# Kernel tuning notes

Hardware: AMD Instinct MI355X
Metric: run time of the kernel (lower is better)

The kernel has to match this reference:

```python
import jax, jax.numpy as jnp
import numpy as np

N = 100000      # num nodes
E = 800000      # num edges
IN = 256        # in_features
D = 64          # out_features per head
H = 4           # num_heads
EF = 64         # edge_feats
NET = 8         # num_etype
SLOPE = 0.2     # leaky relu negative slope


def setup_inputs() -> dict:
    key = jax.random.key(0)
    ks = jax.random.split(key, 12)
    s = 0.05
    h = jax.random.normal(ks[0], (N, IN), jnp.float32)
    row = jax.random.randint(ks[1], (E,), 0, N, dtype=jnp.int32)   # src
    col = jax.random.randint(ks[2], (E,), 0, N, dtype=jnp.int32)   # dst
    tp = jax.random.randint(ks[3], (E,), 0, NET, dtype=jnp.int32)  # edge type
    W = jax.random.normal(ks[4], (IN, D * H), jnp.float32) * s
    W_e = jax.random.normal(ks[5], (EF, EF * H), jnp.float32) * s
    edge_emb = jax.random.normal(ks[6], (NET, EF), jnp.float32) * s
    a_l = jax.random.normal(ks[7], (1, H, D), jnp.float32) * s
    a_r = jax.random.normal(ks[8], (1, H, D), jnp.float32) * s
    a_e = jax.random.normal(ks[9], (1, H, EF), jnp.float32) * s
    res_W = jax.random.normal(ks[10], (IN, D * H), jnp.float32) * s
    res_b = jnp.zeros((D * H,), jnp.float32)
    return {"h": h, "W": W, "W_e": W_e, "edge_emb": edge_emb,
            "a_l": a_l, "a_r": a_r, "a_e": a_e,
            "res_W": res_W, "res_b": res_b,
            "row": row, "col": col, "tp": tp}


def reference(h, W, W_e, edge_emb, a_l, a_r, a_e, res_W, res_b, row, col, tp):
    # node projection -> [N, H, D]; nan-guard as in the original
    emb = jnp.nan_to_num((h @ W).reshape(-1, H, D), nan=0.0)
    # edge-type embedding projection -> [NET, H, EF]
    e = (edge_emb @ W_e).reshape(-1, H, EF)
    # per-edge attention logits [E, H]
    h_l = (a_l * emb).sum(-1)[row]
    h_r = (a_r * emb).sum(-1)[col]
    h_e = (a_e * e).sum(-1)[tp]
    att = jax.nn.leaky_relu(h_l + h_r + h_e, SLOPE)
    # segment softmax over edges grouped by destination node
    m = jax.ops.segment_max(att, col, num_segments=N)          # [N, H]
    ex = jnp.exp(att - m[col])                                 # [E, H]
    denom = jax.ops.segment_sum(ex, col, num_segments=N)      # [N, H]
    alpha = ex / denom[col]                                    # [E, H]
    # gather-multiply-scatter message passing: [E, H, D] -> [N, H, D]
    msg = emb[row] * alpha[:, :, None]
    out = jax.ops.segment_sum(msg, col, num_segments=N).reshape(N, H * D)
    # residual linear + elu activation
    out = out + h @ res_W + res_b
    return jax.nn.elu(out)
```

## Files before the change

kernel.cpp:

```cpp
#include <hip/hip_runtime.h>

#define N_NODES 100000
#define E_EDGES 800000
#define IN_F 256
#define D_HEAD 64
#define H_HEADS 4
#define EF_F 64
#define NET_T 8
#define HD 256
#define SLOPE 0.2f
#define NTILES ((N_NODES + 63) / 64)

typedef unsigned short u16;
typedef unsigned long long u64;
typedef __attribute__((ext_vector_type(8))) short bf16x8;
typedef __attribute__((ext_vector_type(4))) float f32x4;

static __device__ __forceinline__ u16 f2bf(float f) {
    unsigned int u = __float_as_uint(f);
    unsigned int r = u + 0x7FFFu + ((u >> 16) & 1u);
    return (u16)(r >> 16);
}
static __device__ __forceinline__ float bf2f(unsigned int u) {
    return __uint_as_float(u << 16);
}

__global__ void k_se(const float* __restrict__ edge_emb, const float* __restrict__ W_e,
                     const float* __restrict__ a_e, float* __restrict__ s_e) {
    int tid = threadIdx.x;
    int t  = tid >> 5;
    int h  = (tid >> 3) & 3;
    int fc = tid & 7;
    float part = 0.f;
    for (int j = 0; j < 8; ++j) {
        int f = fc * 8 + j;
        float acc = 0.f;
        for (int k = 0; k < EF_F; ++k)
            acc += edge_emb[t * EF_F + k] * W_e[k * (EF_F * H_HEADS) + h * EF_F + f];
        part += a_e[h * EF_F + f] * acc;
    }
    for (int off = 1; off < 8; off <<= 1)
        part += __shfl_xor(part, off, 64);
    if (fc == 0) s_e[t * H_HEADS + h] = part;
}

__global__ void k_prep_w(const float* __restrict__ W, const float* __restrict__ resW,
                         u16* __restrict__ Bfrag) {
    const int gid = blockIdx.x * 256 + threadIdx.x;
    const int lane = gid & 63;
    const int fragid = gid >> 6;
    const int n = fragid & 3;
    const int ks = (fragid >> 2) & 7;
    const int g = fragid >> 5;
    const int c = g * 64 + n * 16 + (lane & 15);
    const int k0 = ks * 32 + (lane >> 4) * 8;
    const float* src = (c < HD) ? &W[c] : &resW[c - HD];
    u16 tmp[8];
#pragma unroll
    for (int j = 0; j < 8; ++j)
        tmp[j] = f2bf(src[(size_t)(k0 + j) * HD]);
    *reinterpret_cast<uint4*>(&Bfrag[(size_t)fragid * 512 + lane * 8]) =
        *reinterpret_cast<const uint4*>(tmp);
}

__global__ __launch_bounds__(512, 2)
void k_mfma(const float* __restrict__ A, const u16* __restrict__ Bfrag,
            const float* __restrict__ a_l, const float* __restrict__ a_r,
            const float* __restrict__ resb,
            u16* __restrict__ emb_bf, float* __restrict__ s_l, float* __restrict__ s_r,
            float* __restrict__ outp) {
    __shared__ char At[32768];
    const int tid = threadIdx.x;
    const int lane = tid & 63;
    const int wid = tid >> 6;
    const int row0 = blockIdx.x * 64;

#pragma unroll
    for (int c = 0; c < 8; ++c) {
        const int lin8 = c * 4096 + tid * 8;
        const int r_lin = lin8 >> 9;
        int grow = row0 + r_lin;
        if (grow >= N_NODES) grow = N_NODES - 1;
        const int colb = lin8 & 511;
        const float4 v = *reinterpret_cast<const float4*>(&A[(size_t)grow * IN_F + (colb >> 1)]);
        uint2 o;
        o.x = (unsigned)f2bf(v.x) | ((unsigned)f2bf(v.y) << 16);
        o.y = (unsigned)f2bf(v.z) | ((unsigned)f2bf(v.w) << 16);
        *reinterpret_cast<uint2*>(&At[lin8 ^ ((r_lin & 7) << 4)]) = o;
    }
    __syncthreads();

    const int lr = lane & 15;
    const int lg = lane >> 4;
    const int xr = (lr & 7) << 4;
    const int klg = lg * 16;

    int rowbase[4];
#pragma unroll
    for (int m = 0; m < 4; ++m) rowbase[m] = (m * 16 + lr) * 512;

    const u16* bp = Bfrag + (size_t)wid * 16384 + lane * 8;

    f32x4 acc[4][4] = {};
#pragma unroll
    for (int ks = 0; ks < 8; ++ks) {
        bf16x8 af[4], bfr[4];
        const int kx = ((ks << 6) + klg) ^ xr;
#pragma unroll
        for (int n = 0; n < 4; ++n)
            bfr[n] = *reinterpret_cast<const bf16x8*>(&bp[ks * 2048 + n * 512]);
#pragma unroll
        for (int m = 0; m < 4; ++m)
            af[m] = *reinterpret_cast<const bf16x8*>(&At[rowbase[m] + kx]);
#pragma unroll
        for (int m = 0; m < 4; ++m)
#pragma unroll
            for (int n = 0; n < 4; ++n)
                acc[m][n] = __builtin_amdgcn_mfma_f32_16x16x32_bf16(bfr[n], af[m], acc[m][n], 0, 0, 0);
    }

    if (wid < 4) {
        const int h = wid;
        float4 alv[4], arv[4];
#pragma unroll
        for (int n = 0; n < 4; ++n) {
            alv[n] = *reinterpret_cast<const float4*>(&a_l[h * D_HEAD + n * 16 + lg * 4]);
            arv[n] = *reinterpret_cast<const float4*>(&a_r[h * D_HEAD + n * 16 + lg * 4]);
        }
#pragma unroll
        for (int m = 0; m < 4; ++m) {
            const int node = row0 + m * 16 + lr;
            float dl = 0.f, dr = 0.f;
            u64 pk[4];
#pragma unroll
            for (int n = 0; n < 4; ++n) {
                float v0 = acc[m][n][0], v1 = acc[m][n][1], v2 = acc[m][n][2], v3 = acc[m][n][3];
                v0 = isnan(v0) ? 0.f : v0;
                v1 = isnan(v1) ? 0.f : v1;
                v2 = isnan(v2) ? 0.f : v2;
                v3 = isnan(v3) ? 0.f : v3;
                dl += v0 * alv[n].x + v1 * alv[n].y + v2 * alv[n].z + v3 * alv[n].w;
                dr += v0 * arv[n].x + v1 * arv[n].y + v2 * arv[n].z + v3 * arv[n].w;
                pk[n] = (u64)f2bf(v0) | ((u64)f2bf(v1) << 16) |
                        ((u64)f2bf(v2) << 32) | ((u64)f2bf(v3) << 48);
            }
            if (node < N_NODES) {
                const size_t base = (size_t)node * HD + h * D_HEAD + lg * 4;
#pragma unroll
                for (int n = 0; n < 4; ++n)
                    *reinterpret_cast<u64*>(&emb_bf[base + n * 16]) = pk[n];
            }
            dl += __shfl_xor(dl, 16, 64); dr += __shfl_xor(dr, 16, 64);
            dl += __shfl_xor(dl, 32, 64); dr += __shfl_xor(dr, 32, 64);
            if (lg == 0 && node < N_NODES) {
                s_l[node * H_HEADS + h] = dl;
                s_r[node * H_HEADS + h] = dr;
            }
        }
    } else {
        const int c0 = (wid - 4) * 64 + lg * 4;
        float4 rb[4];
#pragma unroll
        for (int n = 0; n < 4; ++n)
            rb[n] = *reinterpret_cast<const float4*>(&resb[c0 + n * 16]);
#pragma unroll
        for (int m = 0; m < 4; ++m) {
            const int node = row0 + m * 16 + lr;
            if (node < N_NODES) {
                const size_t base = (size_t)node * HD + c0;
#pragma unroll
                for (int n = 0; n < 4; ++n) {
                    float4 o;
                    o.x = acc[m][n][0] + rb[n].x;
                    o.y = acc[m][n][1] + rb[n].y;
                    o.z = acc[m][n][2] + rb[n].z;
                    o.w = acc[m][n][3] + rb[n].w;
                    *reinterpret_cast<float4*>(&outp[base + n * 16]) = o;
                }
            }
        }
    }
}

__global__ void k_hist(const int* __restrict__ col, int* __restrict__ counts) {
    int e = blockIdx.x * 256 + threadIdx.x;
    if (e < E_EDGES) atomicAdd(&counts[col[e]], 1);
}

__global__ void k_scan1(const int* __restrict__ counts, int* __restrict__ row_ptr,
                        int* __restrict__ partials) {
    __shared__ int sd[256];
    const int t = threadIdx.x, b = blockIdx.x;
    const int base = b * 1024 + t * 4;
    int v[4];
#pragma unroll
    for (int j = 0; j < 4; ++j) v[j] = (base + j < N_NODES) ? counts[base + j] : 0;
    const int s = v[0] + v[1] + v[2] + v[3];
    sd[t] = s;
    __syncthreads();
    for (int off = 1; off < 256; off <<= 1) {
        int y = (t >= off) ? sd[t - off] : 0;
        __syncthreads();
        sd[t] += y;
        __syncthreads();
    }
    int p = sd[t] - s;
#pragma unroll
    for (int j = 0; j < 4; ++j) {
        if (base + j < N_NODES) row_ptr[base + j] = p;
        p += v[j];
    }
    if (t == 255) partials[b] = sd[255];
}

__global__ void k_scan2(int* __restrict__ partials) {
    __shared__ int sd[128];
    const int t = threadIdx.x;
    const int v = (t < 98) ? partials[t] : 0;
    sd[t] = v;
    __syncthreads();
    for (int off = 1; off < 128; off <<= 1) {
        int y = (t >= off) ? sd[t - off] : 0;
        __syncthreads();
        sd[t] += y;
        __syncthreads();
    }
    if (t < 98) partials[t] = sd[t] - v;
}

__global__ void k_scan3(int* __restrict__ row_ptr, int* __restrict__ fill,
                        const int* __restrict__ partials) {
    const int i = blockIdx.x * 256 + threadIdx.x;
    if (i < N_NODES) {
        const int v = row_ptr[i] + partials[i >> 10];
        row_ptr[i] = v;
        fill[i] = v;
    }
    if (i == 0) row_ptr[N_NODES] = E_EDGES;
}

__global__ void k_scatter(const int* __restrict__ row, const int* __restrict__ col,
                          const int* __restrict__ tp, const float* __restrict__ s_l,
                          const float* __restrict__ s_r, const float* __restrict__ s_e,
                          int* __restrict__ fill, int* __restrict__ perm_row,
                          float4* __restrict__ exw_perm) {
    const int e = blockIdx.x * 256 + threadIdx.x;
    if (e >= E_EDGES) return;
    const int r = row[e], c = col[e], t = tp[e];
    const float4 sl = *reinterpret_cast<const float4*>(&s_l[r * 4]);
    const float4 sr = *reinterpret_cast<const float4*>(&s_r[c * 4]);
    const float4 se = *reinterpret_cast<const float4*>(&s_e[t * 4]);
    float4 ex;
    float x;
    x = sl.x + sr.x + se.x; x = (x > 0.f) ? x : SLOPE * x; ex.x = __expf(x);
    x = sl.y + sr.y + se.y; x = (x > 0.f) ? x : SLOPE * x; ex.y = __expf(x);
    x = sl.z + sr.z + se.z; x = (x > 0.f) ? x : SLOPE * x; ex.z = __expf(x);
    x = sl.w + sr.w + se.w; x = (x > 0.f) ? x : SLOPE * x; ex.w = __expf(x);
    const int p = atomicAdd(&fill[c], 1);
    perm_row[p] = r;
    exw_perm[p] = ex;
}

__global__ __launch_bounds__(256)
void k_aggregate(const int* __restrict__ row_ptr, const int* __restrict__ perm_row,
                 const float* __restrict__ exw_perm,
                 const u16* __restrict__ emb_bf, float* __restrict__ outp) {
    const int wave = threadIdx.x >> 6;
    const int lane = threadIdx.x & 63;
    const int n = blockIdx.x * 4 + wave;
    const int h = lane >> 4;
    const int start = row_ptr[n], end = row_ptr[n + 1];
    const size_t o = (size_t)n * HD + lane * 4;
    const float4 res = *reinterpret_cast<const float4*>(&outp[o]);

    float a0 = 0.f, a1 = 0.f, a2 = 0.f, a3 = 0.f, den = 0.f;
    int i = start;
    for (; i + 4 <= end; i += 4) {
        const int r0 = perm_row[i],     r1 = perm_row[i + 1];
        const int r2 = perm_row[i + 2], r3 = perm_row[i + 3];
        const float ex0 = exw_perm[(i)     * 4 + h];
        const float ex1 = exw_perm[(i + 1) * 4 + h];
        const float ex2 = exw_perm[(i + 2) * 4 + h];
        const float ex3 = exw_perm[(i + 3) * 4 + h];
        const u64 ev0 = *reinterpret_cast<const u64*>(&emb_bf[(size_t)r0 * HD + lane * 4]);
        const u64 ev1 = *reinterpret_cast<const u64*>(&emb_bf[(size_t)r1 * HD + lane * 4]);
        const u64 ev2 = *reinterpret_cast<const u64*>(&emb_bf[(size_t)r2 * HD + lane * 4]);
        const u64 ev3 = *reinterpret_cast<const u64*>(&emb_bf[(size_t)r3 * HD + lane * 4]);
        a0 += ex0 * bf2f((unsigned)(ev0) & 0xFFFFu)       + ex1 * bf2f((unsigned)(ev1) & 0xFFFFu)
            + ex2 * bf2f((unsigned)(ev2) & 0xFFFFu)       + ex3 * bf2f((unsigned)(ev3) & 0xFFFFu);
        a1 += ex0 * bf2f((unsigned)(ev0 >> 16) & 0xFFFFu) + ex1 * bf2f((unsigned)(ev1 >> 16) & 0xFFFFu)
            + ex2 * bf2f((unsigned)(ev2 >> 16) & 0xFFFFu) + ex3 * bf2f((unsigned)(ev3 >> 16) & 0xFFFFu);
        a2 += ex0 * bf2f((unsigned)(ev0 >> 32) & 0xFFFFu) + ex1 * bf2f((unsigned)(ev1 >> 32) & 0xFFFFu)
            + ex2 * bf2f((unsigned)(ev2 >> 32) & 0xFFFFu) + ex3 * bf2f((unsigned)(ev3 >> 32) & 0xFFFFu);
        a3 += ex0 * bf2f((unsigned)(ev0 >> 48) & 0xFFFFu) + ex1 * bf2f((unsigned)(ev1 >> 48) & 0xFFFFu)
            + ex2 * bf2f((unsigned)(ev2 >> 48) & 0xFFFFu) + ex3 * bf2f((unsigned)(ev3 >> 48) & 0xFFFFu);
        den += ex0 + ex1 + ex2 + ex3;
    }
    for (; i < end; ++i) {
        const int r0 = perm_row[i];
        const float ex0 = exw_perm[i * 4 + h];
        const u64 ev0 = *reinterpret_cast<const u64*>(&emb_bf[(size_t)r0 * HD + lane * 4]);
        a0 += ex0 * bf2f((unsigned)(ev0) & 0xFFFFu);
        a1 += ex0 * bf2f((unsigned)(ev0 >> 16) & 0xFFFFu);
        a2 += ex0 * bf2f((unsigned)(ev0 >> 32) & 0xFFFFu);
        a3 += ex0 * bf2f((unsigned)(ev0 >> 48) & 0xFFFFu);
        den += ex0;
    }
    const float inv = (den > 0.f) ? 1.f / den : 0.f;
    float4 out;
    float x;
    x = a0 * inv + res.x; out.x = (x > 0.f) ? x : __expf(x) - 1.f;
    x = a1 * inv + res.y; out.y = (x > 0.f) ? x : __expf(x) - 1.f;
    x = a2 * inv + res.z; out.z = (x > 0.f) ? x : __expf(x) - 1.f;
    x = a3 * inv + res.w; out.w = (x > 0.f) ? x : __expf(x) - 1.f;
    *reinterpret_cast<float4*>(&outp[o]) = out;
}

extern "C" void kernel_launch(void* const* d_in, const int* in_sizes, int n_in,
                              void* d_out, int out_size, void* d_ws, size_t ws_size,
                              hipStream_t stream) {
    const float* h    = (const float*)d_in[0];
    const float* W    = (const float*)d_in[1];
    const float* W_e  = (const float*)d_in[2];
    const float* eemb = (const float*)d_in[3];
    const float* a_l  = (const float*)d_in[4];
    const float* a_r  = (const float*)d_in[5];
    const float* a_e  = (const float*)d_in[6];
    const float* resW = (const float*)d_in[7];
    const float* resb = (const float*)d_in[8];
    const int* row = (const int*)d_in[9];
    const int* col = (const int*)d_in[10];
    const int* tp  = (const int*)d_in[11];
    float* outp = (float*)d_out;

    char* ws = (char*)d_ws;
    size_t off = 0;
    auto alloc = [&](size_t b) { size_t o = off; off += (b + 255) & ~(size_t)255; return o; };
    u16*  Bfrag   = (u16*)(ws + alloc((size_t)512 * IN_F * 2));
    u16*  emb_bf  = (u16*)(ws + alloc((size_t)N_NODES * HD * 2));
    float* s_l    = (float*)(ws + alloc((size_t)N_NODES * H_HEADS * 4));
    float* s_r    = (float*)(ws + alloc((size_t)N_NODES * H_HEADS * 4));
    float* s_e    = (float*)(ws + alloc(NET_T * H_HEADS * 4));
    int*  counts  = (int*)(ws + alloc((size_t)N_NODES * 4));
    int*  row_ptr = (int*)(ws + alloc((size_t)(N_NODES + 1) * 4));
    int*  fill    = (int*)(ws + alloc((size_t)N_NODES * 4));
    int*  perm_row= (int*)(ws + alloc((size_t)E_EDGES * 4));
    float* exw_perm=(float*)(ws + alloc((size_t)E_EDGES * H_HEADS * 4));
    int*  partials= (int*)(ws + alloc(128 * 4));

    k_se<<<1, 256, 0, stream>>>(eemb, W_e, a_e, s_e);
    k_prep_w<<<64, 256, 0, stream>>>(W, resW, Bfrag);
    k_mfma<<<NTILES, 512, 0, stream>>>(h, Bfrag, a_l, a_r, resb, emb_bf, s_l, s_r, outp);
    hipMemsetAsync(counts, 0, (size_t)N_NODES * 4, stream);
    k_hist<<<(E_EDGES + 255) / 256, 256, 0, stream>>>(col, counts);
    k_scan1<<<98, 256, 0, stream>>>(counts, row_ptr, partials);
    k_scan2<<<1, 128, 0, stream>>>(partials);
    k_scan3<<<(N_NODES + 255) / 256, 256, 0, stream>>>(row_ptr, fill, partials);
    k_scatter<<<(E_EDGES + 255) / 256, 256, 0, stream>>>(row, col, tp, s_l, s_r, s_e,
                                                         fill, perm_row, (float4*)exw_perm);
    k_aggregate<<<N_NODES / 4, 256, 0, stream>>>(row_ptr, perm_row, exw_perm, emb_bf, outp);
}
```

Before: 311.5 us.

## Store residual projection in bf16 and split MFMA tile across two blocks

The residual linear output is now written as bf16 to a separate workspace buffer instead of fp32 into the output, halving the residual write and re-read traffic in the aggregate kernel. The MFMA kernel is split into two 256-thread blocks per row tile (grid y selects the embedding or residual half), each restaging the full A tile. This raises occupancy granularity but duplicates the load and conversion of the input features, and bf16 rounding of the residual adds precision error.

```diff
diff --git a/kernel.cpp b/kernel.cpp
--- a/kernel.cpp
+++ b/kernel.cpp
@@ -63,21 +63,23 @@
         *reinterpret_cast<const uint4*>(tmp);
 }
 
-__global__ __launch_bounds__(512, 2)
+__global__ __launch_bounds__(256, 4)
 void k_mfma(const float* __restrict__ A, const u16* __restrict__ Bfrag,
             const float* __restrict__ a_l, const float* __restrict__ a_r,
             const float* __restrict__ resb,
             u16* __restrict__ emb_bf, float* __restrict__ s_l, float* __restrict__ s_r,
-            float* __restrict__ outp) {
+            u16* __restrict__ res_bf) {
     __shared__ char At[32768];
     const int tid = threadIdx.x;
     const int lane = tid & 63;
-    const int wid = tid >> 6;
+    const int wv = tid >> 6;
+    const int by = blockIdx.y;
+    const int wid = (by << 2) | wv;
     const int row0 = blockIdx.x * 64;
 
 #pragma unroll
-    for (int c = 0; c < 8; ++c) {
-        const int lin8 = c * 4096 + tid * 8;
+    for (int c = 0; c < 16; ++c) {
+        const int lin8 = c * 2048 + tid * 8;
         const int r_lin = lin8 >> 9;
         int grow = row0 + r_lin;
         if (grow >= N_NODES) grow = N_NODES - 1;
@@ -119,8 +121,8 @@
                 acc[m][n] = __builtin_amdgcn_mfma_f32_16x16x32_bf16(bfr[n], af[m], acc[m][n], 0, 0, 0);
     }
 
-    if (wid < 4) {
-        const int h = wid;
+    if (by == 0) {
+        const int h = wv;
         float4 alv[4], arv[4];
 #pragma unroll
         for (int n = 0; n < 4; ++n) {
@@ -158,7 +160,7 @@
             }
         }
     } else {
-        const int c0 = (wid - 4) * 64 + lg * 4;
+        const int c0 = wv * 64 + lg * 4;
         float4 rb[4];
 #pragma unroll
         for (int n = 0; n < 4; ++n)
@@ -170,12 +172,13 @@
                 const size_t base = (size_t)node * HD + c0;
 #pragma unroll
                 for (int n = 0; n < 4; ++n) {
-                    float4 o;
-                    o.x = acc[m][n][0] + rb[n].x;
-                    o.y = acc[m][n][1] + rb[n].y;
-                    o.z = acc[m][n][2] + rb[n].z;
-                    o.w = acc[m][n][3] + rb[n].w;
-                    *reinterpret_cast<float4*>(&outp[base + n * 16]) = o;
+                    const float v0 = acc[m][n][0] + rb[n].x;
+                    const float v1 = acc[m][n][1] + rb[n].y;
+                    const float v2 = acc[m][n][2] + rb[n].z;
+                    const float v3 = acc[m][n][3] + rb[n].w;
+                    const u64 pk = (u64)f2bf(v0) | ((u64)f2bf(v1) << 16) |
+                                   ((u64)f2bf(v2) << 32) | ((u64)f2bf(v3) << 48);
+                    *reinterpret_cast<u64*>(&res_bf[base + n * 16]) = pk;
                 }
             }
         }
@@ -264,14 +267,15 @@
 __global__ __launch_bounds__(256)
 void k_aggregate(const int* __restrict__ row_ptr, const int* __restrict__ perm_row,
                  const float* __restrict__ exw_perm,
-                 const u16* __restrict__ emb_bf, float* __restrict__ outp) {
+                 const u16* __restrict__ emb_bf, const u16* __restrict__ res_bf,
+                 float* __restrict__ outp) {
     const int wave = threadIdx.x >> 6;
     const int lane = threadIdx.x & 63;
     const int n = blockIdx.x * 4 + wave;
     const int h = lane >> 4;
     const int start = row_ptr[n], end = row_ptr[n + 1];
     const size_t o = (size_t)n * HD + lane * 4;
-    const float4 res = *reinterpret_cast<const float4*>(&outp[o]);
+    const u64 rv = *reinterpret_cast<const u64*>(&res_bf[o]);
 
     float a0 = 0.f, a1 = 0.f, a2 = 0.f, a3 = 0.f, den = 0.f;
     int i = start;
@@ -309,10 +313,10 @@
     const float inv = (den > 0.f) ? 1.f / den : 0.f;
     float4 out;
     float x;
-    x = a0 * inv + res.x; out.x = (x > 0.f) ? x : __expf(x) - 1.f;
-    x = a1 * inv + res.y; out.y = (x > 0.f) ? x : __expf(x) - 1.f;
-    x = a2 * inv + res.z; out.z = (x > 0.f) ? x : __expf(x) - 1.f;
-    x = a3 * inv + res.w; out.w = (x > 0.f) ? x : __expf(x) - 1.f;
+    x = a0 * inv + bf2f((unsigned)(rv) & 0xFFFFu);       out.x = (x > 0.f) ? x : __expf(x) - 1.f;
+    x = a1 * inv + bf2f((unsigned)(rv >> 16) & 0xFFFFu); out.y = (x > 0.f) ? x : __expf(x) - 1.f;
+    x = a2 * inv + bf2f((unsigned)(rv >> 32) & 0xFFFFu); out.z = (x > 0.f) ? x : __expf(x) - 1.f;
+    x = a3 * inv + bf2f((unsigned)(rv >> 48) & 0xFFFFu); out.w = (x > 0.f) ? x : __expf(x) - 1.f;
     *reinterpret_cast<float4*>(&outp[o]) = out;
 }
 
@@ -338,6 +342,7 @@
     auto alloc = [&](size_t b) { size_t o = off; off += (b + 255) & ~(size_t)255; return o; };
     u16*  Bfrag   = (u16*)(ws + alloc((size_t)512 * IN_F * 2));
     u16*  emb_bf  = (u16*)(ws + alloc((size_t)N_NODES * HD * 2));
+    u16*  res_bf  = (u16*)(ws + alloc((size_t)N_NODES * HD * 2));
     float* s_l    = (float*)(ws + alloc((size_t)N_NODES * H_HEADS * 4));
     float* s_r    = (float*)(ws + alloc((size_t)N_NODES * H_HEADS * 4));
     float* s_e    = (float*)(ws + alloc(NET_T * H_HEADS * 4));
@@ -350,7 +355,8 @@
 
     k_se<<<1, 256, 0, stream>>>(eemb, W_e, a_e, s_e);
     k_prep_w<<<64, 256, 0, stream>>>(W, resW, Bfrag);
-    k_mfma<<<NTILES, 512, 0, stream>>>(h, Bfrag, a_l, a_r, resb, emb_bf, s_l, s_r, outp);
+    dim3 g2(NTILES, 2);
+    k_mfma<<<g2, 256, 0, stream>>>(h, Bfrag, a_l, a_r, resb, emb_bf, s_l, s_r, res_bf);
     hipMemsetAsync(counts, 0, (size_t)N_NODES * 4, stream);
     k_hist<<<(E_EDGES + 255) / 256, 256, 0, stream>>>(col, counts);
     k_scan1<<<98, 256, 0, stream>>>(counts, row_ptr, partials);
@@ -358,5 +364,5 @@
     k_scan3<<<(N_NODES + 255) / 256, 256, 0, stream>>>(row_ptr, fill, partials);
     k_scatter<<<(E_EDGES + 255) / 256, 256, 0, stream>>>(row, col, tp, s_l, s_r, s_e,
                                                          fill, perm_row, (float4*)exw_perm);
-    k_aggregate<<<N_NODES / 4, 256, 0, stream>>>(row_ptr, perm_row, exw_perm, emb_bf, outp);
-}
+    k_aggregate<<<N_NODES / 4, 256, 0, stream>>>(row_ptr, perm_row, exw_perm, emb_bf, res_bf, outp);
+}
```

New measurement: 308.7 us. Within noise of the previous version (-0.9%).
